# Kernel optimization log

Measured on AMD Instinct MI355X. Metric: run time of the kernel, lower is better.

Reference implementation:

```python
import jax, jax.numpy as jnp
import numpy as np


def setup_inputs() -> dict:
    key = jax.random.key(0)
    k1, k2, k3 = jax.random.split(key, 3)
    B, S, D = 4, 2048, 1024   # batch, seq_len, hidden
    M = 65536                 # external memory size
    x = jax.random.normal(k1, (B, S, D), dtype=jnp.float32)
    keys = jax.random.normal(k2, (M, D), dtype=jnp.float32)
    vals = jax.random.normal(k3, (M, D), dtype=jnp.float32)
    return {"x": x, "ver": 1, "keys": keys, "vals": vals}


def reference(x, ver, keys, vals):
    # linear_attention: unnormalized attention over external memory.
    #   out = (x @ keys^T) @ vals
    # Use associativity to avoid materializing the [B,S,M] score matrix:
    #   kv = keys^T @ vals  -> [D, D]
    kv = jnp.einsum("md,me->de", keys, vals)   # [D, D]
    out = jnp.einsum("bsd,de->bse", x, kv)      # [B, S, D]
    return out
```

## Files before the change

### kernel.cpp

```cpp
#include <hip/hip_runtime.h>
#include <hip/hip_bf16.h>


typedef __attribute__((ext_vector_type(8))) __bf16 bf16x8;
typedef __attribute__((ext_vector_type(4))) __bf16 bf16x4;
typedef __attribute__((ext_vector_type(4))) float  f32x4;

#define D_DIM   1024
#define M_DIM   65536
#define ROWS    8192
#define NCHUNK  16
#define MC      (M_DIM / NCHUNK)
#define BT      128
#define BK      64
#define LDK     72
#define TILE_BYTES 16384

__device__ __forceinline__ f32x4 mfma16(bf16x8 a, bf16x8 b, f32x4 c) {
    return __builtin_amdgcn_mfma_f32_16x16x32_bf16(a, b, c, 0, 0, 0);
}

__device__ __forceinline__ void gl_lds16(const void* gsrc, void* ldst) {
    __builtin_amdgcn_global_load_lds(
        (const __attribute__((address_space(1))) unsigned int*)gsrc,
        (__attribute__((address_space(3))) unsigned int*)ldst,
        16, 0, 0);
}

__global__ __launch_bounds__(256)
void convert_tile(const float* __restrict__ keys,
                  const float* __restrict__ vals,
                  __hip_bfloat16* __restrict__ KtT,
                  __hip_bfloat16* __restrict__ VtT)
{
    __shared__ __bf16 Lt[128][72];

    const float* src = blockIdx.z ? vals : keys;
    char* dstb = (char*)(blockIdx.z ? VtT : KtT);

    const int tid = threadIdx.x;
    const int s  = blockIdx.x;
    const int t  = blockIdx.y;
    const int m0 = s * 64;
    const int d0 = t * 128;

    #pragma unroll
    for (int i = 0; i < 8; ++i) {
        const int idx = tid + i * 256;
        const int mr  = idx >> 5;
        const int dc  = (idx & 31) * 4;
        f32x4 v = *(const f32x4*)(src + (size_t)(m0 + mr) * D_DIM + d0 + dc);
        #pragma unroll
        for (int j = 0; j < 4; ++j)
            Lt[dc + j][mr] = (__bf16)v[j];
    }
    __syncthreads();

    char* dst_tile = dstb + ((size_t)t * 1024 + s) * TILE_BYTES;
    #pragma unroll
    for (int r = 0; r < 4; ++r) {
        const int o  = r * 4096 + tid * 16;
        const int dl = o >> 7;
        const int c  = (o >> 4) & 7;
        const int cl = c ^ (dl & 7);
        bf16x8 w = *(const bf16x8*)&Lt[dl][cl * 8];
        *(bf16x8*)(dst_tile + o) = w;
    }
}

__global__ __launch_bounds__(256)
void kv_gemm(const __hip_bfloat16* __restrict__ VtT,
             const __hip_bfloat16* __restrict__ KtT,
             float* __restrict__ kvw)
{
    __shared__ __bf16 Va[2][128][64];
    __shared__ __bf16 Ka[2][128][64];

    const int tid  = threadIdx.x;
    const int lane = tid & 63;
    const int wave = tid >> 6;
    const int wr   = wave >> 1;
    const int wc   = wave & 1;

    const int i64   = blockIdx.x & 63;
    const int chunk = blockIdx.x >> 6;
    const int xcd   = i64 & 7;
    const int slot  = i64 >> 3;
    const int e8 = (xcd >> 1) * 2 + (slot >> 2);
    const int d8 = (xcd & 1) * 4 + (slot & 3);

    const char* srcV = (const char*)VtT
        + ((size_t)e8 * 1024 + (size_t)chunk * 64) * TILE_BYTES
        + wave * 4096 + lane * 16;
    const char* srcK = (const char*)KtT
        + ((size_t)d8 * 1024 + (size_t)chunk * 64) * TILE_BYTES
        + wave * 4096 + lane * 16;

    f32x4 acc[4][4] = {};

    const int l15 = lane & 15;
    const int l7  = lane & 7;
    const int hi  = lane >> 4;

    auto stage = [&](int buf, int t) {
        const char* sv = srcV + (size_t)t * TILE_BYTES;
        const char* sk = srcK + (size_t)t * TILE_BYTES;
        char* dv = (char*)&Va[buf][0][0] + wave * 4096;
        char* dk = (char*)&Ka[buf][0][0] + wave * 4096;
        #pragma unroll
        for (int i = 0; i < 4; ++i) {
            gl_lds16(sv + i * 1024, dv + i * 1024);
            gl_lds16(sk + i * 1024, dk + i * 1024);
        }
    };

    stage(0, 0);

    for (int t = 0; t < 64; ++t) {
        if (t + 1 < 64) {
            stage((t + 1) & 1, t + 1);
            asm volatile("s_waitcnt vmcnt(8)" ::: "memory");
        } else {
            asm volatile("s_waitcnt vmcnt(0)" ::: "memory");
        }
        __builtin_amdgcn_s_barrier();

        const char* vbase = (const char*)&Va[t & 1][0][0];
        const char* kbase = (const char*)&Ka[t & 1][0][0];
        #pragma unroll
        for (int ks = 0; ks < BK; ks += 32) {
            bf16x8 af[4], bf[4];
            const int ca = (ks >> 3) + hi;
            const int pc = (ca ^ l7) << 4;
            #pragma unroll
            for (int tt = 0; tt < 4; ++tt) {
                const int ra = wr * 64 + tt * 16 + l15;
                const int rb = wc * 64 + tt * 16 + l15;
                af[tt] = *(const bf16x8*)(vbase + ra * 128 + pc);
                bf[tt] = *(const bf16x8*)(kbase + rb * 128 + pc);
            }
            #pragma unroll
            for (int mi = 0; mi < 4; ++mi)
                #pragma unroll
                for (int ni = 0; ni < 4; ++ni)
                    acc[mi][ni] = mfma16(af[mi], bf[ni], acc[mi][ni]);
        }
        __builtin_amdgcn_s_barrier();
    }

    const int rbase = (lane >> 4) * 4;
    const int cidx  = lane & 15;
    #pragma unroll
    for (int mi = 0; mi < 4; ++mi) {
        #pragma unroll
        for (int ni = 0; ni < 4; ++ni) {
            const int d = d8 * BT + wc * 64 + ni * 16 + cidx;
            #pragma unroll
            for (int reg = 0; reg < 4; ++reg) {
                const int e = e8 * BT + wr * 64 + mi * 16 + rbase + reg;
                atomicAdd(kvw + (size_t)e * D_DIM + d, acc[mi][ni][reg]);
            }
        }
    }
}

__global__ __launch_bounds__(256)
void kv_partial_kernel(const float* __restrict__ keys,
                       const float* __restrict__ vals,
                       float* __restrict__ kvw)
{
    __shared__ __bf16 Ktl[BT][LDK];
    __shared__ __bf16 Vtl[BT][LDK];

    const int tid  = threadIdx.x;
    const int lane = tid & 63;
    const int wave = tid >> 6;
    const int wr   = wave >> 1;
    const int wc   = wave & 1;

    const int tile  = blockIdx.x & 63;
    const int chunk = blockIdx.x >> 6;
    const int d0 = (tile >> 3) * BT;
    const int e0 = (tile & 7) * BT;
    const size_t mbeg = (size_t)chunk * MC;

    f32x4 acc[4][4] = {};
    const int kg  = tid & 15;
    const int d4a = tid >> 4;

    for (int ms = 0; ms < MC; ms += BK) {
        #pragma unroll
        for (int i = 0; i < 2; ++i) {
            const int dloc = (d4a + i * 16) * 4;
            const size_t mrow = mbeg + ms + (size_t)kg * 4;
            f32x4 kr[4], vr[4];
            #pragma unroll
            for (int r = 0; r < 4; ++r) {
                kr[r] = *(const f32x4*)(keys + (mrow + r) * D_DIM + d0 + dloc);
                vr[r] = *(const f32x4*)(vals + (mrow + r) * D_DIM + e0 + dloc);
            }
            #pragma unroll
            for (int j = 0; j < 4; ++j) {
                bf16x4 wk, wv;
                #pragma unroll
                for (int r = 0; r < 4; ++r) {
                    wk[r] = (__bf16)kr[r][j];
                    wv[r] = (__bf16)vr[r][j];
                }
                *(bf16x4*)&Ktl[dloc + j][kg * 4] = wk;
                *(bf16x4*)&Vtl[dloc + j][kg * 4] = wv;
            }
        }
        __syncthreads();

        #pragma unroll
        for (int ks = 0; ks < BK; ks += 32) {
            bf16x8 af[4], bf[4];
            #pragma unroll
            for (int t = 0; t < 4; ++t) {
                af[t] = *(const bf16x8*)&Ktl[wr * 64 + t * 16 + (lane & 15)][ks + (lane >> 4) * 8];
                bf[t] = *(const bf16x8*)&Vtl[wc * 64 + t * 16 + (lane & 15)][ks + (lane >> 4) * 8];
            }
            #pragma unroll
            for (int mi = 0; mi < 4; ++mi)
                #pragma unroll
                for (int ni = 0; ni < 4; ++ni)
                    acc[mi][ni] = mfma16(af[mi], bf[ni], acc[mi][ni]);
        }
        __syncthreads();
    }

    const int rbase = (lane >> 4) * 4;
    const int cidx  = lane & 15;
    #pragma unroll
    for (int mi = 0; mi < 4; ++mi) {
        #pragma unroll
        for (int ni = 0; ni < 4; ++ni) {
            const int e = e0 + wc * 64 + ni * 16 + cidx;
            #pragma unroll
            for (int reg = 0; reg < 4; ++reg) {
                const int d = d0 + wr * 64 + mi * 16 + rbase + reg;
                atomicAdd(kvw + (size_t)e * D_DIM + d, acc[mi][ni][reg]);
            }
        }
    }
}

__global__ __launch_bounds__(256)
void out_gemm_kernel(const float* __restrict__ x,
                     const float* __restrict__ kvw,
                     float* __restrict__ out)
{
    __shared__ __bf16 Xt[BT][LDK];
    __shared__ __bf16 Wt[BT][LDK];

    const int tid  = threadIdx.x;
    const int lane = tid & 63;
    const int wave = tid >> 6;
    const int wr   = wave >> 1;
    const int wc   = wave & 1;

    const int r0 = blockIdx.x * BT;
    const int e0 = blockIdx.y * BT;

    f32x4 acc[4][4] = {};

    for (int ks0 = 0; ks0 < D_DIM; ks0 += BK) {
        #pragma unroll
        for (int i = 0; i < 8; ++i) {
            const int idx = tid + i * 256;
            const int row = idx >> 4;
            const int col = (idx & 15) * 4;
            f32x4 xa = *(const f32x4*)(x   + (size_t)(r0 + row) * D_DIM + ks0 + col);
            f32x4 wa = *(const f32x4*)(kvw + (size_t)(e0 + row) * D_DIM + ks0 + col);
            bf16x4 xb, wb;
            #pragma unroll
            for (int j = 0; j < 4; ++j) {
                xb[j] = (__bf16)xa[j];
                wb[j] = (__bf16)wa[j];
            }
            *(bf16x4*)&Xt[row][col] = xb;
            *(bf16x4*)&Wt[row][col] = wb;
        }
        __syncthreads();

        #pragma unroll
        for (int ks = 0; ks < BK; ks += 32) {
            bf16x8 af[4], bf[4];
            #pragma unroll
            for (int t = 0; t < 4; ++t) {
                af[t] = *(const bf16x8*)&Xt[wr * 64 + t * 16 + (lane & 15)][ks + (lane >> 4) * 8];
                bf[t] = *(const bf16x8*)&Wt[wc * 64 + t * 16 + (lane & 15)][ks + (lane >> 4) * 8];
            }
            #pragma unroll
            for (int mi = 0; mi < 4; ++mi)
                #pragma unroll
                for (int ni = 0; ni < 4; ++ni)
                    acc[mi][ni] = mfma16(af[mi], bf[ni], acc[mi][ni]);
        }
        __syncthreads();
    }

    const int rbase = (lane >> 4) * 4;
    const int cidx  = lane & 15;
    #pragma unroll
    for (int mi = 0; mi < 4; ++mi) {
        #pragma unroll
        for (int ni = 0; ni < 4; ++ni) {
            const int e = e0 + wc * 64 + ni * 16 + cidx;
            #pragma unroll
            for (int reg = 0; reg < 4; ++reg) {
                const int r = r0 + wr * 64 + mi * 16 + rbase + reg;
                out[(size_t)r * D_DIM + e] = acc[mi][ni][reg];
            }
        }
    }
}

extern "C" void kernel_launch(void* const* d_in, const int* in_sizes, int n_in,
                              void* d_out, int out_size, void* d_ws, size_t ws_size,
                              hipStream_t stream) {
    const float* x    = (const float*)d_in[0];
    const float* keys = (const float*)d_in[2];
    const float* vals = (const float*)d_in[3];
    float* out = (float*)d_out;

    const size_t kvw_bytes = (size_t)D_DIM * D_DIM * sizeof(float);
    const size_t kt_bytes  = (size_t)D_DIM * M_DIM * sizeof(__hip_bfloat16);
    const size_t need      = kvw_bytes + 2 * kt_bytes;

    float* kvw = (float*)d_ws;
    hipMemsetAsync(kvw, 0, kvw_bytes, stream);

    if (ws_size >= need) {
        __hip_bfloat16* KtT = (__hip_bfloat16*)((char*)d_ws + kvw_bytes);
        __hip_bfloat16* VtT = (__hip_bfloat16*)((char*)d_ws + kvw_bytes + kt_bytes);
        convert_tile<<<dim3(M_DIM / 64, D_DIM / 128, 2), dim3(256), 0, stream>>>(
            keys, vals, KtT, VtT);
        kv_gemm<<<dim3(64 * NCHUNK), dim3(256), 0, stream>>>(VtT, KtT, kvw);
    } else {
        kv_partial_kernel<<<dim3(64 * NCHUNK), dim3(256), 0, stream>>>(keys, vals, kvw);
    }
    out_gemm_kernel<<<dim3(64, 8), dim3(256), 0, stream>>>(x, kvw, out);
}
```

Baseline: 437.5 us.

## Use 256x256 output tiles with 8-wave blocks and interleaved prefetch in kv GEMM

Replaces the 128x128-tile, 4-wave kv GEMM with a 256x256-tile, 8-wave kernel. Each block now covers one M-chunk of 64 steps across a 256x256 output tile, with a remapped XCD-aware chunk assignment and 256 blocks instead of 1024. Global-to-LDS prefetch of the next tile is interleaved between MFMA phases, and s_setprio raises priority around the MFMA bursts. The goal is higher arithmetic intensity per LDS byte and fewer atomic adds to the output. The cost is more registers (8x4 accumulators) and a grid of only 256 blocks, which could leave the GPU underused.

```diff
diff --git a/kernel.cpp b/kernel.cpp
--- a/kernel.cpp
+++ b/kernel.cpp
@@ -68,97 +68,122 @@
     }
 }
 
-__global__ __launch_bounds__(256)
-void kv_gemm(const __hip_bfloat16* __restrict__ VtT,
-             const __hip_bfloat16* __restrict__ KtT,
-             float* __restrict__ kvw)
+__global__ __launch_bounds__(512, 2)
+void kv_gemm8(const __hip_bfloat16* __restrict__ VtT,
+              const __hip_bfloat16* __restrict__ KtT,
+              float* __restrict__ kvw)
 {
-    __shared__ __bf16 Va[2][128][64];
-    __shared__ __bf16 Ka[2][128][64];
+    __shared__ __align__(16) char lds[2][4][TILE_BYTES];
 
     const int tid  = threadIdx.x;
     const int lane = tid & 63;
     const int wave = tid >> 6;
-    const int wr   = wave >> 1;
-    const int wc   = wave & 1;
-
-    const int i64   = blockIdx.x & 63;
-    const int chunk = blockIdx.x >> 6;
-    const int xcd   = i64 & 7;
-    const int slot  = i64 >> 3;
-    const int e8 = (xcd >> 1) * 2 + (slot >> 2);
-    const int d8 = (xcd & 1) * 4 + (slot & 3);
-
-    const char* srcV = (const char*)VtT
-        + ((size_t)e8 * 1024 + (size_t)chunk * 64) * TILE_BYTES
-        + wave * 4096 + lane * 16;
-    const char* srcK = (const char*)KtT
-        + ((size_t)d8 * 1024 + (size_t)chunk * 64) * TILE_BYTES
-        + wave * 4096 + lane * 16;
-
-    f32x4 acc[4][4] = {};
+    const int we   = wave >> 2;
+    const int wd   = wave & 3;
+
+    const int bx    = blockIdx.x;
+    const int xcd   = bx & 7;
+    const int idx   = bx >> 3;
+    const int chunk = ((idx >> 4) << 3) | xcd;
+    const int t16   = idx & 15;
+    const int E8    = t16 >> 2;
+    const int D8    = t16 & 3;
+
+    const size_t step0 = (size_t)chunk * 64;
+
+    const char* Vb = (const char*)VtT;
+    const char* Kb = (const char*)KtT;
 
     const int l15 = lane & 15;
     const int l7  = lane & 7;
     const int hi  = lane >> 4;
 
-    auto stage = [&](int buf, int t) {
-        const char* sv = srcV + (size_t)t * TILE_BYTES;
-        const char* sk = srcK + (size_t)t * TILE_BYTES;
-        char* dv = (char*)&Va[buf][0][0] + wave * 4096;
-        char* dk = (char*)&Ka[buf][0][0] + wave * 4096;
-        #pragma unroll
-        for (int i = 0; i < 4; ++i) {
-            gl_lds16(sv + i * 1024, dv + i * 1024);
-            gl_lds16(sk + i * 1024, dk + i * 1024);
-        }
+    f32x4 acc[8][4] = {};
+
+    auto tileptr = [&](const char* base, int rt, int t) -> const char* {
+        return base + ((size_t)rt * 1024 + step0 + (size_t)t) * TILE_BYTES;
     };
-
-    stage(0, 0);
-
+    auto stage_sub = [&](int buf, int sub, const char* tile) {
+        char* dst = &lds[buf][sub][wave * 1024];
+        const char* s = tile + wave * 1024 + lane * 16;
+        gl_lds16(s,        dst);
+        gl_lds16(s + 8192, dst + 8192);
+    };
+
+    stage_sub(0, 0, tileptr(Vb, 2 * E8,     0));
+    stage_sub(0, 1, tileptr(Vb, 2 * E8 + 1, 0));
+    stage_sub(0, 2, tileptr(Kb, 2 * D8,     0));
+    stage_sub(0, 3, tileptr(Kb, 2 * D8 + 1, 0));
+    asm volatile("s_waitcnt vmcnt(0)" ::: "memory");
+    __builtin_amdgcn_s_barrier();
+
+    bf16x8 bfr[4][2];
+
+    #pragma unroll 2
     for (int t = 0; t < 64; ++t) {
-        if (t + 1 < 64) {
-            stage((t + 1) & 1, t + 1);
-            asm volatile("s_waitcnt vmcnt(8)" ::: "memory");
-        } else {
-            asm volatile("s_waitcnt vmcnt(0)" ::: "memory");
-        }
-        __builtin_amdgcn_s_barrier();
-
-        const char* vbase = (const char*)&Va[t & 1][0][0];
-        const char* kbase = (const char*)&Ka[t & 1][0][0];
-        #pragma unroll
-        for (int ks = 0; ks < BK; ks += 32) {
-            bf16x8 af[4], bf[4];
-            const int ca = (ks >> 3) + hi;
-            const int pc = (ca ^ l7) << 4;
-            #pragma unroll
-            for (int tt = 0; tt < 4; ++tt) {
-                const int ra = wr * 64 + tt * 16 + l15;
-                const int rb = wc * 64 + tt * 16 + l15;
-                af[tt] = *(const bf16x8*)(vbase + ra * 128 + pc);
-                bf[tt] = *(const bf16x8*)(kbase + rb * 128 + pc);
-            }
-            #pragma unroll
-            for (int mi = 0; mi < 4; ++mi)
-                #pragma unroll
-                for (int ni = 0; ni < 4; ++ni)
-                    acc[mi][ni] = mfma16(af[mi], bf[ni], acc[mi][ni]);
-        }
-        __builtin_amdgcn_s_barrier();
-    }
-
-    const int rbase = (lane >> 4) * 4;
-    const int cidx  = lane & 15;
-    #pragma unroll
-    for (int mi = 0; mi < 4; ++mi) {
+        const int buf = t & 1;
+        const char* abase = &lds[buf][we][0];
+        const char* bbase = &lds[buf][2 + (wd >> 1)][0];
+        const int brow0 = (wd & 1) * 64;
+
+        #pragma unroll
+        for (int p = 0; p < 4; ++p) {
+            bf16x8 afr[2][2];
+            #pragma unroll
+            for (int j = 0; j < 2; ++j)
+                #pragma unroll
+                for (int ks = 0; ks < 2; ++ks) {
+                    const int row = (2 * p + j) * 16 + l15;
+                    afr[j][ks] = *(const bf16x8*)(abase + row * 128
+                                   + (((ks << 2) + hi) ^ l7) * 16);
+                }
+            if (p == 0) {
+                #pragma unroll
+                for (int n = 0; n < 4; ++n)
+                    #pragma unroll
+                    for (int ks = 0; ks < 2; ++ks) {
+                        const int row = brow0 + n * 16 + l15;
+                        bfr[n][ks] = *(const bf16x8*)(bbase + row * 128
+                                       + (((ks << 2) + hi) ^ l7) * 16);
+                    }
+            }
+            if (p == 0 && t + 1 < 64) {
+                stage_sub(buf ^ 1, 0, tileptr(Vb, 2 * E8,     t + 1));
+                stage_sub(buf ^ 1, 1, tileptr(Vb, 2 * E8 + 1, t + 1));
+            }
+            if (p == 1 && t + 1 < 64) {
+                stage_sub(buf ^ 1, 2, tileptr(Kb, 2 * D8,     t + 1));
+                stage_sub(buf ^ 1, 3, tileptr(Kb, 2 * D8 + 1, t + 1));
+            }
+            __builtin_amdgcn_s_barrier();
+            asm volatile("s_waitcnt lgkmcnt(0)" ::: "memory");
+            __builtin_amdgcn_sched_barrier(0);
+            __builtin_amdgcn_s_setprio(1);
+            #pragma unroll
+            for (int j = 0; j < 2; ++j)
+                #pragma unroll
+                for (int n = 0; n < 4; ++n)
+                    #pragma unroll
+                    for (int ks = 0; ks < 2; ++ks)
+                        acc[2 * p + j][n] = mfma16(afr[j][ks], bfr[n][ks],
+                                                   acc[2 * p + j][n]);
+            __builtin_amdgcn_s_setprio(0);
+            if (p == 3)
+                asm volatile("s_waitcnt vmcnt(0)" ::: "memory");
+            __builtin_amdgcn_s_barrier();
+        }
+    }
+
+    const int rb = hi * 4;
+    #pragma unroll
+    for (int mi = 0; mi < 8; ++mi) {
         #pragma unroll
         for (int ni = 0; ni < 4; ++ni) {
-            const int d = d8 * BT + wc * 64 + ni * 16 + cidx;
-            #pragma unroll
-            for (int reg = 0; reg < 4; ++reg) {
-                const int e = e8 * BT + wr * 64 + mi * 16 + rbase + reg;
-                atomicAdd(kvw + (size_t)e * D_DIM + d, acc[mi][ni][reg]);
+            const int d = D8 * 256 + wd * 64 + ni * 16 + l15;
+            #pragma unroll
+            for (int r = 0; r < 4; ++r) {
+                const int e = E8 * 256 + we * 128 + mi * 16 + rb + r;
+                atomicAdd(kvw + (size_t)e * D_DIM + d, acc[mi][ni][r]);
             }
         }
     }
@@ -337,7 +362,7 @@
         __hip_bfloat16* VtT = (__hip_bfloat16*)((char*)d_ws + kvw_bytes + kt_bytes);
         convert_tile<<<dim3(M_DIM / 64, D_DIM / 128, 2), dim3(256), 0, stream>>>(
             keys, vals, KtT, VtT);
-        kv_gemm<<<dim3(64 * NCHUNK), dim3(256), 0, stream>>>(VtT, KtT, kvw);
+        kv_gemm8<<<dim3(256), dim3(512), 0, stream>>>(VtT, KtT, kvw);
     } else {
         kv_partial_kernel<<<dim3(64 * NCHUNK), dim3(256), 0, stream>>>(keys, vals, kvw);
     }
```

Result: faster. 366.9 us (-16.1%).
